# Kernel optimization log

Hardware: AMD Instinct MI355X
Metric: run time of the kernel (lower is better)

The kernel has to match this reference:

```python
import jax, jax.numpy as jnp
import numpy as np

DIM = 128
H = W = 56
NUM_HEADS = 4
WS = 7            # window size
SHIFT = 3
N = WS * WS       # tokens per window (49)
EPS = 1e-5


def _relative_position_index():
    coords = np.stack(np.meshgrid(np.arange(WS), np.arange(WS), indexing='ij'))  # [2,ws,ws]
    cf = coords.reshape(2, -1)                                                   # [2,N]
    rel = cf[:, :, None] - cf[:, None, :]                                        # [2,N,N]
    rel = rel.transpose(1, 2, 0).astype(np.int64)                                # [N,N,2]
    rel[:, :, 0] += WS - 1
    rel[:, :, 1] += WS - 1
    rel[:, :, 0] *= 2 * WS - 1
    return rel.sum(-1)  # [N,N]


def _attn_mask():
    # shifted-window attention mask, [nW, N, N] with 0 / -100
    img = np.zeros((H, W), dtype=np.float32)
    cnt = 0
    for hs in (slice(0, -WS), slice(-WS, -SHIFT), slice(-SHIFT, None)):
        for ws_ in (slice(0, -WS), slice(-WS, -SHIFT), slice(-SHIFT, None)):
            img[hs, ws_] = cnt
            cnt += 1
    mw = img.reshape(H // WS, WS, W // WS, WS).transpose(0, 2, 1, 3).reshape(-1, N)  # [nW,N]
    diff = mw[:, None, :] - mw[:, :, None]
    return np.where(diff != 0, -100.0, 0.0).astype(np.float32)


_RPI = jnp.asarray(_relative_position_index())
_MASK = jnp.asarray(_attn_mask())


def _layernorm(x, g, b):
    mu = jnp.mean(x, axis=-1, keepdims=True)
    var = jnp.mean(jnp.square(x - mu), axis=-1, keepdims=True)
    return (x - mu) * jax.lax.rsqrt(var + EPS) * g + b


def _window_partition(x):
    # x: [B,H,W,C] -> [B*nW, N, C]
    B, _, _, C = x.shape
    x = x.reshape(B, H // WS, WS, W // WS, WS, C).transpose(0, 1, 3, 2, 4, 5)
    return x.reshape(-1, N, C)


def _window_reverse(w, B):
    # [B*nW, N, C] -> [B,H,W,C]
    C = w.shape[-1]
    x = w.reshape(B, H // WS, W // WS, WS, WS, C).transpose(0, 1, 3, 2, 4, 5)
    return x.reshape(B, H, W, C)


def setup_inputs() -> dict:
    key = jax.random.key(0)
    ks = jax.random.split(key, 8)
    B, L, C = 64, H * W, DIM
    hid = 4 * DIM
    s = 0.02
    return {
        'x': jax.random.normal(ks[0], (B, L, C), jnp.float32),
        'norm1_g': jnp.ones((C,), jnp.float32),
        'norm1_b': jnp.zeros((C,), jnp.float32),
        'qkv_w': jax.random.normal(ks[1], (C, 3 * C), jnp.float32) * s,
        'qkv_b': jnp.zeros((3 * C,), jnp.float32),
        'rel_bias_table': jax.random.normal(ks[2], ((2 * WS - 1) ** 2, NUM_HEADS), jnp.float32) * s,
        'proj_w': jax.random.normal(ks[3], (C, C), jnp.float32) * s,
        'proj_b': jnp.zeros((C,), jnp.float32),
        'norm2_g': jnp.ones((C,), jnp.float32),
        'norm2_b': jnp.zeros((C,), jnp.float32),
        'fc1_w': jax.random.normal(ks[4], (C, hid), jnp.float32) * s,
        'fc1_b': jnp.zeros((hid,), jnp.float32),
        'fc2_w': jax.random.normal(ks[5], (hid, C), jnp.float32) * s,
        'fc2_b': jnp.zeros((C,), jnp.float32),
    }


def reference(x, norm1_g, norm1_b, qkv_w, qkv_b, rel_bias_table, proj_w, proj_b,
              norm2_g, norm2_b, fc1_w, fc1_b, fc2_w, fc2_b):
    B, L, C = x.shape
    hdim = C // NUM_HEADS
    scale = hdim ** -0.5

    shortcut = x
    xn = _layernorm(x, norm1_g, norm1_b).reshape(B, H, W, C)

    # cyclic shift (H,W divisible by WS -> no padding)
    xs = jnp.roll(xn, shift=(-SHIFT, -SHIFT), axis=(1, 2))
    xw = _window_partition(xs)                      # [B*nW, N, C]
    B_ = xw.shape[0]
    nW = B_ // B

    # window attention
    qkv = xw @ qkv_w + qkv_b                        # [B_,N,3C]
    qkv = qkv.reshape(B_, N, 3, NUM_HEADS, hdim).transpose(2, 0, 3, 1, 4)
    q, k, v = qkv[0], qkv[1], qkv[2]                # [B_,h,N,d]
    attn = jnp.einsum('bhnd,bhmd->bhnm', q * scale, k)
    bias = rel_bias_table[_RPI.reshape(-1)].reshape(N, N, NUM_HEADS)
    attn = attn + bias.transpose(2, 0, 1)[None]
    attn = attn.reshape(B, nW, NUM_HEADS, N, N) + _MASK[None, :, None]
    attn = jax.nn.softmax(attn.reshape(B_, NUM_HEADS, N, N), axis=-1)
    out = jnp.einsum('bhnm,bhmd->bhnd', attn, v)
    out = out.transpose(0, 2, 1, 3).reshape(B_, N, C)
    out = out @ proj_w + proj_b

    # reverse windows, un-shift
    xr = _window_reverse(out, B)
    xr = jnp.roll(xr, shift=(SHIFT, SHIFT), axis=(1, 2))
    x = shortcut + xr.reshape(B, L, C)

    # MLP with exact GELU (torch nn.GELU default)
    xn2 = _layernorm(x, norm2_g, norm2_b)
    h = jax.nn.gelu(xn2 @ fc1_w + fc1_b, approximate=False)
    x = x + (h @ fc2_w + fc2_b)
    return x
```

## Files before the change

kernel.cpp:

```cpp
#include <hip/hip_runtime.h>
#include <cstdint>

#define DIM   128
#define NH    4
#define WSZ   7
#define NTOK  49
#define SHIFT 3
#define HIMG  56
#define BATCH 64
#define LTOK  3136
#define HID   512
#define EPSF  1e-5f

typedef short bf16x8 __attribute__((ext_vector_type(8)));
typedef float f32x4  __attribute__((ext_vector_type(4)));

__device__ __forceinline__ float bf2f(ushort u){ return __uint_as_float(((uint32_t)u)<<16); }
__device__ __forceinline__ ushort f2bf(float f){
  uint32_t u = __float_as_uint(f);
  u += 0x7FFFu + ((u>>16)&1u);
  return (ushort)(u>>16);
}

__device__ __forceinline__ float gelu_f(float v){
  float xa = fabsf(v) * 0.70710678118654752f;
  float t  = __builtin_amdgcn_rcpf(fmaf(0.3275911f, xa, 1.0f));
  float p  = fmaf(fmaf(fmaf(fmaf(1.061405429f, t, -1.453152027f), t,
                       1.421413741f), t, -0.284496736f), t, 0.254829592f) * t;
  float e  = __expf(-xa*xa);
  float er = copysignf(fmaf(-p, e, 1.0f), v);
  return 0.5f * v * (1.0f + er);
}

__global__ __launch_bounds__(256) void transpose_cvt_all(
    const float* __restrict__ qkvw, const float* __restrict__ pw,
    const float* __restrict__ f1w,  const float* __restrict__ f2w,
    ushort* __restrict__ ws)
{
  __shared__ ushort tile[32][33];
  int bid = blockIdx.x;
  const float* src; ushort* dst; int R, Cc, b0;
  if (bid < 48)       { src = qkvw; dst = ws;          R = 128; Cc = 384; b0 = 0;   }
  else if (bid < 64)  { src = pw;   dst = ws + 49152;  R = 128; Cc = 128; b0 = 48;  }
  else if (bid < 128) { src = f1w;  dst = ws + 65536;  R = 128; Cc = 512; b0 = 64;  }
  else                { src = f2w;  dst = ws + 131072; R = 512; Cc = 128; b0 = 128; }
  int t = bid - b0;
  int tpr = Cc >> 5;
  int tr = t / tpr, tc = t % tpr;
  int tx = threadIdx.x & 31, ty = threadIdx.x >> 5;
  #pragma unroll
  for (int k = 0; k < 4; k++){
    int r = tr*32 + ty + k*8;
    tile[ty + k*8][tx] = f2bf(src[(size_t)r*Cc + tc*32 + tx]);
  }
  __syncthreads();
  #pragma unroll
  for (int k = 0; k < 4; k++){
    int c = tc*32 + ty + k*8;
    dst[(size_t)c*R + tr*32 + tx] = tile[tx][ty + k*8];
  }
}

#define OFF_BUFA 0
#define OFF_QK   8704
#define QKSTR    40
#define OFF_TBL  (OFF_QK + 8*NTOK*QKSTR)
#define OFF_PP   (OFF_QK + 12936)
#define SMEM_SZ  25072

__global__ __launch_bounds__(256,3) void swin_block_kernel(
    const float* __restrict__ x, const float* __restrict__ n1g, const float* __restrict__ n1b,
    const ushort* __restrict__ qkv_wt, const float* __restrict__ qkvb,
    const float* __restrict__ bias_tbl, const ushort* __restrict__ proj_wt,
    const float* __restrict__ projb,
    const float* __restrict__ n2g, const float* __restrict__ n2b,
    const ushort* __restrict__ fc1_wt, const float* __restrict__ fc1b,
    const ushort* __restrict__ fc2_wt, const float* __restrict__ fc2b,
    float* __restrict__ out)
{
  __shared__ ushort smem[SMEM_SZ];

  const int tid  = threadIdx.x;
  const int wave = tid >> 6;
  const int lane = tid & 63;
  const int b_   = blockIdx.x;
  const int b    = b_ >> 6;
  const int win  = b_ & 63;
  const int wi   = win >> 3, wj = win & 7;

  const int ncol  = lane & 15;
  const int quad  = lane >> 4;
  const int koff  = quad * 8;
  const int rbase = quad * 4;
  const int l32   = lane & 31;
  const int hlf   = lane >> 5;

  for (int i = tid; i < 676; i += 256) smem[OFF_TBL + i] = f2bf(bias_tbl[i]);

  {
    const int c = l32*4;
    const float4 g4 = *(const float4*)(n1g + c);
    const float4 b4 = *(const float4*)(n1b + c);
    for (int r = wave*2 + hlf; r < NTOK; r += 8){
      int ti = r / 7, tj = r % 7;
      int hh = (wi*7 + ti + SHIFT) % HIMG;
      int ww = (wj*7 + tj + SHIFT) % HIMG;
      float4 tv = *(const float4*)(x + ((size_t)b*LTOK + hh*HIMG + ww)*DIM + c);
      float sm = tv.x + tv.y + tv.z + tv.w;
      #pragma unroll
      for (int off=16; off; off>>=1) sm += __shfl_xor(sm, off, 64);
      float mu = sm * (1.0f/128.0f);
      float d0 = tv.x-mu, d1 = tv.y-mu, d2 = tv.z-mu, d3 = tv.w-mu;
      float sq = d0*d0 + d1*d1 + d2*d2 + d3*d3;
      #pragma unroll
      for (int off=16; off; off>>=1) sq += __shfl_xor(sq, off, 64);
      float rstd = rsqrtf(sq*(1.0f/128.0f) + EPSF);
      ushort4 o;
      o.x = f2bf(d0*rstd*g4.x + b4.x);
      o.y = f2bf(d1*rstd*g4.y + b4.y);
      o.z = f2bf(d2*rstd*g4.z + b4.z);
      o.w = f2bf(d3*rstd*g4.w + b4.w);
      *(ushort4*)&smem[OFF_BUFA + r*136 + c] = o;
    }
  }
  __syncthreads();

  {
    bf16x8 afrag[4][4];
    #pragma unroll
    for (int mt=0; mt<4; mt++)
      #pragma unroll
      for (int kb=0; kb<4; kb++)
        afrag[mt][kb] = *(const bf16x8*)&smem[OFF_BUFA + (mt*16 + ncol)*136 + kb*32 + koff];
    __syncthreads();

    for (int i = tid; i < 128*15; i += 256){
      int dd = i/15, t = 49 + i%15;
      smem[OFF_BUFA + dd*68 + t] = 0;
    }

    #pragma unroll
    for (int nt=0; nt<6; nt++){
      int c = wave*96 + nt*16 + ncol;
      int which = c >> 7, head = (c >> 5) & 3, d = c & 31;
      bf16x8 bfrag[4];
      #pragma unroll
      for (int kb=0; kb<4; kb++) bfrag[kb] = *(const bf16x8*)(qkv_wt + (size_t)c*128 + kb*32 + koff);
      float bias = qkvb[c];
      int qkb = OFF_QK + (head*2 + which)*NTOK*QKSTR + d;
      int vb  = OFF_BUFA + (head*32 + d)*68;
      #pragma unroll
      for (int mt=0; mt<4; mt++){
        f32x4 acc = {0.f,0.f,0.f,0.f};
        #pragma unroll
        for (int kb=0; kb<4; kb++)
          acc = __builtin_amdgcn_mfma_f32_16x16x32_bf16(afrag[mt][kb], bfrag[kb], acc, 0,0,0);
        #pragma unroll
        for (int r=0; r<4; r++){
          int m = mt*16 + rbase + r;
          if (m < NTOK){
            ushort v = f2bf(acc[r] + bias);
            if (which == 2) smem[vb + m] = v;
            else            smem[qkb + m*QKSTR] = v;
          }
        }
      }
    }
  }
  __syncthreads();

  float4 xpre[7];

  {
    const int h = wave;
    const int qbase = OFF_QK + (h*2    )*NTOK*QKSTR;
    const int kbase = OFF_QK + (h*2 + 1)*NTOK*QKSTR;
    const int pbase = qbase;

    bf16x8 qf[4], kf[4];
    #pragma unroll
    for (int mt=0; mt<4; mt++) qf[mt] = *(const bf16x8*)&smem[qbase + (mt*16 + ncol)*QKSTR + koff];
    #pragma unroll
    for (int nt=0; nt<4; nt++) kf[nt] = *(const bf16x8*)&smem[kbase + (nt*16 + ncol)*QKSTR + koff];

    f32x4 s[4][4];
    #pragma unroll
    for (int mt=0; mt<4; mt++)
      #pragma unroll
      for (int nt=0; nt<4; nt++){
        f32x4 z = {0.f,0.f,0.f,0.f};
        s[mt][nt] = __builtin_amdgcn_mfma_f32_16x16x32_bf16(qf[mt], kf[nt], z, 0,0,0);
      }

    int kcol[4], rm[4];
    #pragma unroll
    for (int nt=0; nt<4; nt++){
      int k = nt*16 + ncol;
      kcol[nt] = k;
      int kc = k < NTOK ? k : 48;
      int si = kc/7, sj = kc%7;
      int sh = wi*7 + si, sw = wj*7 + sj;
      rm[nt] = (sh<49?0:(sh<53?1:2))*3 + (sw<49?0:(sw<53?1:2));
    }
    const float scale = 0.17677669529663687f;

    #pragma unroll
    for (int mt=0; mt<4; mt++){
      #pragma unroll
      for (int r=0; r<4; r++){
        int m  = mt*16 + rbase + r;
        int mc = m < NTOK ? m : 48;
        int ti = mc/7, tj = mc%7;
        int habs = wi*7 + ti, wabs = wj*7 + tj;
        int rn = (habs<49?0:(habs<53?1:2))*3 + (wabs<49?0:(wabs<53?1:2));
        float sv[4];
        #pragma unroll
        for (int nt=0; nt<4; nt++){
          int k  = kcol[nt];
          int kc = k < NTOK ? k : 48;
          int si = kc/7, sj = kc%7;
          int idx = (ti - si + 6)*13 + (tj - sj + 6);
          float bias = bf2f(smem[OFF_TBL + idx*4 + h]);
          float v = s[mt][nt][r]*scale + bias + (rn == rm[nt] ? 0.f : -100.f);
          sv[nt] = (k < NTOK) ? v : -1e30f;
        }
        float sum = 0.f;
        #pragma unroll
        for (int nt=0; nt<4; nt++){ sv[nt] = __expf(sv[nt]); sum += sv[nt]; }
        #pragma unroll
        for (int off=1; off<16; off<<=1) sum += __shfl_xor(sum, off, 64);
        float rs = 1.0f/sum;
        #pragma unroll
        for (int nt=0; nt<4; nt++) s[mt][nt][r] = sv[nt]*rs;
      }
    }

    #pragma unroll
    for (int kk=0; kk<7; kk++){
      int rr = wave*2 + hlf + kk*8;
      if (rr < NTOK){
        int ti = rr/7, tj = rr%7;
        int hh = (wi*7 + ti + SHIFT) % HIMG;
        int ww = (wj*7 + tj + SHIFT) % HIMG;
        xpre[kk] = *(const float4*)(x + ((size_t)b*LTOK + hh*HIMG + ww)*DIM + l32*4);
      }
    }

    #pragma unroll
    for (int mt=0; mt<4; mt++)
      #pragma unroll
      for (int r=0; r<4; r++){
        int m = mt*16 + rbase + r;
        if (m < NTOK){
          #pragma unroll
          for (int nt=0; nt<4; nt++)
            smem[pbase + m*72 + kcol[nt]] = f2bf(s[mt][nt][r]);
        }
      }

    bf16x8 vf[2][2];
    #pragma unroll
    for (int nt=0; nt<2; nt++)
      #pragma unroll
      for (int kq=0; kq<2; kq++)
        vf[nt][kq] = *(const bf16x8*)&smem[OFF_BUFA + (h*32 + nt*16 + ncol)*68 + kq*32 + koff];
    __syncthreads();

    f32x4 o[4][2];
    #pragma unroll
    for (int mt=0; mt<4; mt++)
      #pragma unroll
      for (int nt=0; nt<2; nt++){ f32x4 z={0.f,0.f,0.f,0.f}; o[mt][nt]=z; }

    #pragma unroll
    for (int mt=0; mt<4; mt++)
      #pragma unroll
      for (int kq=0; kq<2; kq++){
        bf16x8 pf = *(const bf16x8*)&smem[pbase + (mt*16 + ncol)*72 + kq*32 + koff];
        #pragma unroll
        for (int nt=0; nt<2; nt++)
          o[mt][nt] = __builtin_amdgcn_mfma_f32_16x16x32_bf16(pf, vf[nt][kq], o[mt][nt], 0,0,0);
      }

    #pragma unroll
    for (int mt=0; mt<4; mt++)
      #pragma unroll
      for (int nt=0; nt<2; nt++)
        #pragma unroll
        for (int r=0; r<4; r++){
          int m = mt*16 + rbase + r;
          if (m < NTOK)
            smem[OFF_BUFA + m*136 + h*32 + nt*16 + ncol] = f2bf(o[mt][nt][r]);
        }
  }
  __syncthreads();

  float* xstage = (float*)&smem[OFF_QK];
  #pragma unroll
  for (int kk=0; kk<7; kk++){
    int rr = wave*2 + hlf + kk*8;
    if (rr < NTOK) *(float4*)&xstage[rr*132 + l32*4] = xpre[kk];
  }

  float x2reg[2][4][4];
  {
    bf16x8 afrag[4][4];
    #pragma unroll
    for (int mt=0; mt<4; mt++)
      #pragma unroll
      for (int kb=0; kb<4; kb++)
        afrag[mt][kb] = *(const bf16x8*)&smem[OFF_BUFA + (mt*16 + ncol)*136 + kb*32 + koff];
    __syncthreads();

    #pragma unroll
    for (int nt=0; nt<2; nt++){
      int j = wave*32 + nt*16 + ncol;
      bf16x8 bfrag[4];
      #pragma unroll
      for (int kb=0; kb<4; kb++) bfrag[kb] = *(const bf16x8*)(proj_wt + (size_t)j*128 + kb*32 + koff);
      float bias = projb[j];
      #pragma unroll
      for (int mt=0; mt<4; mt++){
        f32x4 acc = {0.f,0.f,0.f,0.f};
        #pragma unroll
        for (int kb=0; kb<4; kb++)
          acc = __builtin_amdgcn_mfma_f32_16x16x32_bf16(afrag[mt][kb], bfrag[kb], acc, 0,0,0);
        #pragma unroll
        for (int r=0; r<4; r++){
          int m = mt*16 + rbase + r;
          if (m < NTOK) x2reg[nt][mt][r] = acc[r] + bias + xstage[m*132 + j];
          else          x2reg[nt][mt][r] = 0.f;
        }
      }
    }
  }

  float2* pp = (float2*)&smem[OFF_PP];
  #pragma unroll
  for (int mt=0; mt<4; mt++)
    #pragma unroll
    for (int r=0; r<4; r++){
      float a0 = x2reg[0][mt][r], a1 = x2reg[1][mt][r];
      float sm = a0 + a1, sq = a0*a0 + a1*a1;
      #pragma unroll
      for (int off=1; off<16; off<<=1){ sm += __shfl_xor(sm, off, 64); sq += __shfl_xor(sq, off, 64); }
      if (ncol == 0) pp[(mt*16 + rbase + r)*4 + wave] = make_float2(sm, sq);
    }
  __syncthreads();

  {
    const int j0 = wave*32 + ncol, j1 = j0 + 16;
    const float g0 = n2g[j0], be0 = n2b[j0], g1 = n2g[j1], be1 = n2b[j1];
    #pragma unroll
    for (int mt=0; mt<4; mt++)
      #pragma unroll
      for (int r=0; r<4; r++){
        int m = mt*16 + rbase + r;
        f32x4 pa = *(const f32x4*)&pp[m*4];
        f32x4 pb = *(const f32x4*)&pp[m*4 + 2];
        float sm = pa[0]+pa[2]+pb[0]+pb[2];
        float sq = pa[1]+pa[3]+pb[1]+pb[3];
        float mu   = sm * (1.0f/128.0f);
        float rstd = rsqrtf(sq*(1.0f/128.0f) - mu*mu + EPSF);
        smem[OFF_BUFA + m*136 + j0] = f2bf((x2reg[0][mt][r]-mu)*rstd*g0 + be0);
        smem[OFF_BUFA + m*136 + j1] = f2bf((x2reg[1][mt][r]-mu)*rstd*g1 + be1);
      }
  }
  __syncthreads();

  f32x4 o2[2][4];
  #pragma unroll
  for (int nt=0; nt<2; nt++)
    #pragma unroll
    for (int mt=0; mt<4; mt++){ f32x4 z={0.f,0.f,0.f,0.f}; o2[nt][mt]=z; }

  for (int hk=0; hk<4; hk++){
    {
      bf16x8 bfrag2[2][4];
      float  bias2[2];
      #pragma unroll
      for (int nt=0; nt<2; nt++){
        int c = hk*128 + wave*32 + nt*16 + ncol;
        #pragma unroll
        for (int kb=0; kb<4; kb++)
          bfrag2[nt][kb] = *(const bf16x8*)(fc1_wt + (size_t)c*128 + kb*32 + koff);
        bias2[nt] = fc1b[c];
      }
      #pragma unroll
      for (int mt=0; mt<4; mt++){
        bf16x8 a4[4];
        #pragma unroll
        for (int kb=0; kb<4; kb++)
          a4[kb] = *(const bf16x8*)&smem[OFF_BUFA + (mt*16 + ncol)*136 + kb*32 + koff];
        #pragma unroll
        for (int nt=0; nt<2; nt++){
          f32x4 acc = {0.f,0.f,0.f,0.f};
          #pragma unroll
          for (int kb=0; kb<4; kb++)
            acc = __builtin_amdgcn_mfma_f32_16x16x32_bf16(a4[kb], bfrag2[nt][kb], acc, 0,0,0);
          int cloc = wave*32 + nt*16 + ncol;
          #pragma unroll
          for (int r=0; r<4; r++){
            int m = mt*16 + rbase + r;
            if (mt < 3 || m < NTOK)
              smem[OFF_QK + m*136 + cloc] = f2bf(gelu_f(acc[r] + bias2[nt]));
          }
        }
      }
    }
    __syncthreads();

    {
      bf16x8 bfrag2[2][4];
      #pragma unroll
      for (int nt=0; nt<2; nt++){
        int j = wave*32 + nt*16 + ncol;
        #pragma unroll
        for (int kb=0; kb<4; kb++)
          bfrag2[nt][kb] = *(const bf16x8*)(fc2_wt + (size_t)j*512 + hk*128 + kb*32 + koff);
      }
      #pragma unroll
      for (int mt=0; mt<4; mt++){
        bf16x8 ha4[4];
        #pragma unroll
        for (int kb=0; kb<4; kb++)
          ha4[kb] = *(const bf16x8*)&smem[OFF_QK + (mt*16 + ncol)*136 + kb*32 + koff];
        #pragma unroll
        for (int nt=0; nt<2; nt++)
          #pragma unroll
          for (int kb=0; kb<4; kb++)
            o2[nt][mt] = __builtin_amdgcn_mfma_f32_16x16x32_bf16(ha4[kb], bfrag2[nt][kb], o2[nt][mt], 0,0,0);
      }
    }
    __syncthreads();
  }

  float* fout = (float*)&smem[OFF_QK];
  #pragma unroll
  for (int nt=0; nt<2; nt++){
    int j = wave*32 + nt*16 + ncol;
    float bias = fc2b[j];
    #pragma unroll
    for (int mt=0; mt<4; mt++){
      #pragma unroll
      for (int r=0; r<4; r++){
        int m = mt*16 + rbase + r;
        if (m < NTOK)
          fout[m*132 + j] = o2[nt][mt][r] + bias + x2reg[nt][mt][r];
      }
    }
  }
  __syncthreads();

  for (int rr = wave*2 + hlf; rr < NTOK; rr += 8){
    int ti = rr/7, tj = rr%7;
    int hh = (wi*7 + ti + SHIFT) % HIMG;
    int ww = (wj*7 + tj + SHIFT) % HIMG;
    float4 v = *(const float4*)&fout[rr*132 + l32*4];
    *(float4*)(out + ((size_t)b*LTOK + hh*HIMG + ww)*DIM + l32*4) = v;
  }
}

extern "C" void kernel_launch(void* const* d_in, const int* in_sizes, int n_in,
                              void* d_out, int out_size, void* d_ws, size_t ws_size,
                              hipStream_t stream)
{
  const float* x    = (const float*)d_in[0];
  const float* n1g  = (const float*)d_in[1];
  const float* n1b  = (const float*)d_in[2];
  const float* qkvw = (const float*)d_in[3];
  const float* qkvb = (const float*)d_in[4];
  const float* tbl  = (const float*)d_in[5];
  const float* pw   = (const float*)d_in[6];
  const float* pb   = (const float*)d_in[7];
  const float* n2g  = (const float*)d_in[8];
  const float* n2b  = (const float*)d_in[9];
  const float* f1w  = (const float*)d_in[10];
  const float* f1b  = (const float*)d_in[11];
  const float* f2w  = (const float*)d_in[12];
  const float* f2b  = (const float*)d_in[13];

  ushort* wsbase = (ushort*)d_ws;
  transpose_cvt_all<<<192, 256, 0, stream>>>(qkvw, pw, f1w, f2w, wsbase);

  swin_block_kernel<<<4096, 256, 0, stream>>>(x, n1g, n1b, wsbase, qkvb, tbl,
                                              wsbase + 49152, pb, n2g, n2b,
                                              wsbase + 65536, f1b, wsbase + 131072, f2b,
                                              (float*)d_out);
}
```

Measured before the change: 486.9 us.

## Prefetch weight fragments early and simplify softmax bias/exp computation

Global weight fragments for the QKV, proj, fc1 and fc2 GEMMs are now loaded ahead of use: before barriers, one tile ahead in loops, or at the start of each MLP chunk. This hides global-load latency behind MFMA work and synchronisation. The relative-position bias table is stored in fp32 prescaled by log2(e), so softmax uses a single fma and exp2 with a precomputed index offset instead of per-element index arithmetic and bf16 decode. The residual x prefetch is moved before the softmax. The cost is more live registers under launch_bounds(256,3), which risks spills, plus slightly more shared memory.

```diff
diff --git a/kernel.cpp b/kernel.cpp
--- a/kernel.cpp
+++ b/kernel.cpp
@@ -15,7 +15,6 @@
 typedef short bf16x8 __attribute__((ext_vector_type(8)));
 typedef float f32x4  __attribute__((ext_vector_type(4)));
 
-__device__ __forceinline__ float bf2f(ushort u){ return __uint_as_float(((uint32_t)u)<<16); }
 __device__ __forceinline__ ushort f2bf(float f){
   uint32_t u = __float_as_uint(f);
   u += 0x7FFFu + ((u>>16)&1u);
@@ -66,7 +65,7 @@
 #define QKSTR    40
 #define OFF_TBL  (OFF_QK + 8*NTOK*QKSTR)
 #define OFF_PP   (OFF_QK + 12936)
-#define SMEM_SZ  25072
+#define SMEM_SZ  25744
 
 __global__ __launch_bounds__(256,3) void swin_block_kernel(
     const float* __restrict__ x, const float* __restrict__ n1g, const float* __restrict__ n1b,
@@ -95,7 +94,10 @@
   const int l32   = lane & 31;
   const int hlf   = lane >> 5;
 
-  for (int i = tid; i < 676; i += 256) smem[OFF_TBL + i] = f2bf(bias_tbl[i]);
+  {
+    float* tblI = (float*)&smem[OFF_TBL];
+    for (int i = tid; i < 676; i += 256) tblI[i] = bias_tbl[i] * 1.4426950408889634f;
+  }
 
   {
     const int c = l32*4;
@@ -123,6 +125,14 @@
       *(ushort4*)&smem[OFF_BUFA + r*136 + c] = o;
     }
   }
+
+  bf16x8 bfp[4];
+  {
+    int c0 = wave*96 + ncol;
+    #pragma unroll
+    for (int kb=0; kb<4; kb++)
+      bfp[kb] = *(const bf16x8*)(qkv_wt + (size_t)c0*128 + kb*32 + koff);
+  }
   __syncthreads();
 
   {
@@ -142,10 +152,16 @@
     #pragma unroll
     for (int nt=0; nt<6; nt++){
       int c = wave*96 + nt*16 + ncol;
+      bf16x8 bfrag[4];
+      #pragma unroll
+      for (int kb=0; kb<4; kb++) bfrag[kb] = bfp[kb];
+      if (nt < 5){
+        int cn = c + 16;
+        #pragma unroll
+        for (int kb=0; kb<4; kb++)
+          bfp[kb] = *(const bf16x8*)(qkv_wt + (size_t)cn*128 + kb*32 + koff);
+      }
       int which = c >> 7, head = (c >> 5) & 3, d = c & 31;
-      bf16x8 bfrag[4];
-      #pragma unroll
-      for (int kb=0; kb<4; kb++) bfrag[kb] = *(const bf16x8*)(qkv_wt + (size_t)c*128 + kb*32 + koff);
       float bias = qkvb[c];
       int qkb = OFF_QK + (head*2 + which)*NTOK*QKSTR + d;
       int vb  = OFF_BUFA + (head*32 + d)*68;
@@ -192,7 +208,18 @@
         s[mt][nt] = __builtin_amdgcn_mfma_f32_16x16x32_bf16(qf[mt], kf[nt], z, 0,0,0);
       }
 
-    int kcol[4], rm[4];
+    #pragma unroll
+    for (int kk=0; kk<7; kk++){
+      int rr = wave*2 + hlf + kk*8;
+      if (rr < NTOK){
+        int ti = rr/7, tj = rr%7;
+        int hh = (wi*7 + ti + SHIFT) % HIMG;
+        int ww = (wj*7 + tj + SHIFT) % HIMG;
+        xpre[kk] = *(const float4*)(x + ((size_t)b*LTOK + hh*HIMG + ww)*DIM + l32*4);
+      }
+    }
+
+    int kcol[4], rm[4], offI[4];
     #pragma unroll
     for (int nt=0; nt<4; nt++){
       int k = nt*16 + ncol;
@@ -201,8 +228,11 @@
       int si = kc/7, sj = kc%7;
       int sh = wi*7 + si, sw = wj*7 + sj;
       rm[nt] = (sh<49?0:(sh<53?1:2))*3 + (sw<49?0:(sw<53?1:2));
-    }
-    const float scale = 0.17677669529663687f;
+      offI[nt] = (si*13 + sj)*4;
+    }
+    const float* tblF = (const float*)&smem[OFF_TBL];
+    const float SCL2 = 0.25503486f;
+    const float MASK_L2E = -144.26950408889634f;
 
     #pragma unroll
     for (int mt=0; mt<4; mt++){
@@ -213,36 +243,22 @@
         int ti = mc/7, tj = mc%7;
         int habs = wi*7 + ti, wabs = wj*7 + tj;
         int rn = (habs<49?0:(habs<53?1:2))*3 + (wabs<49?0:(wabs<53?1:2));
+        int baseI = (ti*13 + tj + 84)*4 + h;
         float sv[4];
         #pragma unroll
         for (int nt=0; nt<4; nt++){
-          int k  = kcol[nt];
-          int kc = k < NTOK ? k : 48;
-          int si = kc/7, sj = kc%7;
-          int idx = (ti - si + 6)*13 + (tj - sj + 6);
-          float bias = bf2f(smem[OFF_TBL + idx*4 + h]);
-          float v = s[mt][nt][r]*scale + bias + (rn == rm[nt] ? 0.f : -100.f);
-          sv[nt] = (k < NTOK) ? v : -1e30f;
+          float bias = tblF[baseI - offI[nt]];
+          float v = fmaf(s[mt][nt][r], SCL2, bias) + (rn == rm[nt] ? 0.f : MASK_L2E);
+          sv[nt] = (kcol[nt] < NTOK) ? v : -1e30f;
         }
         float sum = 0.f;
         #pragma unroll
-        for (int nt=0; nt<4; nt++){ sv[nt] = __expf(sv[nt]); sum += sv[nt]; }
+        for (int nt=0; nt<4; nt++){ sv[nt] = __builtin_amdgcn_exp2f(sv[nt]); sum += sv[nt]; }
         #pragma unroll
         for (int off=1; off<16; off<<=1) sum += __shfl_xor(sum, off, 64);
         float rs = 1.0f/sum;
         #pragma unroll
         for (int nt=0; nt<4; nt++) s[mt][nt][r] = sv[nt]*rs;
-      }
-    }
-
-    #pragma unroll
-    for (int kk=0; kk<7; kk++){
-      int rr = wave*2 + hlf + kk*8;
-      if (rr < NTOK){
-        int ti = rr/7, tj = rr%7;
-        int hh = (wi*7 + ti + SHIFT) % HIMG;
-        int ww = (wj*7 + tj + SHIFT) % HIMG;
-        xpre[kk] = *(const float4*)(x + ((size_t)b*LTOK + hh*HIMG + ww)*DIM + l32*4);
       }
     }
 
@@ -302,6 +318,15 @@
     if (rr < NTOK) *(float4*)&xstage[rr*132 + l32*4] = xpre[kk];
   }
 
+  bf16x8 pbf[2][4];
+  #pragma unroll
+  for (int nt=0; nt<2; nt++){
+    int j = wave*32 + nt*16 + ncol;
+    #pragma unroll
+    for (int kb=0; kb<4; kb++)
+      pbf[nt][kb] = *(const bf16x8*)(proj_wt + (size_t)j*128 + kb*32 + koff);
+  }
+
   float x2reg[2][4][4];
   {
     bf16x8 afrag[4][4];
@@ -315,16 +340,13 @@
     #pragma unroll
     for (int nt=0; nt<2; nt++){
       int j = wave*32 + nt*16 + ncol;
-      bf16x8 bfrag[4];
-      #pragma unroll
-      for (int kb=0; kb<4; kb++) bfrag[kb] = *(const bf16x8*)(proj_wt + (size_t)j*128 + kb*32 + koff);
       float bias = projb[j];
       #pragma unroll
       for (int mt=0; mt<4; mt++){
         f32x4 acc = {0.f,0.f,0.f,0.f};
         #pragma unroll
         for (int kb=0; kb<4; kb++)
-          acc = __builtin_amdgcn_mfma_f32_16x16x32_bf16(afrag[mt][kb], bfrag[kb], acc, 0,0,0);
+          acc = __builtin_amdgcn_mfma_f32_16x16x32_bf16(afrag[mt][kb], pbf[nt][kb], acc, 0,0,0);
         #pragma unroll
         for (int r=0; r<4; r++){
           int m = mt*16 + rbase + r;
@@ -347,6 +369,15 @@
       if (ncol == 0) pp[(mt*16 + rbase + r)*4 + wave] = make_float2(sm, sq);
     }
   __syncthreads();
+
+  bf16x8 f1p[2][4];
+  #pragma unroll
+  for (int nt=0; nt<2; nt++){
+    int c = wave*32 + nt*16 + ncol;
+    #pragma unroll
+    for (int kb=0; kb<4; kb++)
+      f1p[nt][kb] = *(const bf16x8*)(fc1_wt + (size_t)c*128 + kb*32 + koff);
+  }
 
   {
     const int j0 = wave*32 + ncol, j1 = j0 + 16;
@@ -375,17 +406,19 @@
     for (int mt=0; mt<4; mt++){ f32x4 z={0.f,0.f,0.f,0.f}; o2[nt][mt]=z; }
 
   for (int hk=0; hk<4; hk++){
+    bf16x8 f2p[2][4];
+    #pragma unroll
+    for (int nt=0; nt<2; nt++){
+      int j = wave*32 + nt*16 + ncol;
+      #pragma unroll
+      for (int kb=0; kb<4; kb++)
+        f2p[nt][kb] = *(const bf16x8*)(fc2_wt + (size_t)j*512 + hk*128 + kb*32 + koff);
+    }
+
     {
-      bf16x8 bfrag2[2][4];
-      float  bias2[2];
-      #pragma unroll
-      for (int nt=0; nt<2; nt++){
-        int c = hk*128 + wave*32 + nt*16 + ncol;
-        #pragma unroll
-        for (int kb=0; kb<4; kb++)
-          bfrag2[nt][kb] = *(const bf16x8*)(fc1_wt + (size_t)c*128 + kb*32 + koff);
-        bias2[nt] = fc1b[c];
-      }
+      float bias2[2];
+      #pragma unroll
+      for (int nt=0; nt<2; nt++) bias2[nt] = fc1b[hk*128 + wave*32 + nt*16 + ncol];
       #pragma unroll
       for (int mt=0; mt<4; mt++){
         bf16x8 a4[4];
@@ -397,7 +430,7 @@
           f32x4 acc = {0.f,0.f,0.f,0.f};
           #pragma unroll
           for (int kb=0; kb<4; kb++)
-            acc = __builtin_amdgcn_mfma_f32_16x16x32_bf16(a4[kb], bfrag2[nt][kb], acc, 0,0,0);
+            acc = __builtin_amdgcn_mfma_f32_16x16x32_bf16(a4[kb], f1p[nt][kb], acc, 0,0,0);
           int cloc = wave*32 + nt*16 + ncol;
           #pragma unroll
           for (int r=0; r<4; r++){
@@ -408,29 +441,28 @@
         }
       }
     }
+    if (hk < 3){
+      #pragma unroll
+      for (int nt=0; nt<2; nt++){
+        int c = (hk+1)*128 + wave*32 + nt*16 + ncol;
+        #pragma unroll
+        for (int kb=0; kb<4; kb++)
+          f1p[nt][kb] = *(const bf16x8*)(fc1_wt + (size_t)c*128 + kb*32 + koff);
+      }
+    }
     __syncthreads();
 
-    {
-      bf16x8 bfrag2[2][4];
-      #pragma unroll
-      for (int nt=0; nt<2; nt++){
-        int j = wave*32 + nt*16 + ncol;
+    #pragma unroll
+    for (int mt=0; mt<4; mt++){
+      bf16x8 ha4[4];
+      #pragma unroll
+      for (int kb=0; kb<4; kb++)
+        ha4[kb] = *(const bf16x8*)&smem[OFF_QK + (mt*16 + ncol)*136 + kb*32 + koff];
+      #pragma unroll
+      for (int nt=0; nt<2; nt++)
         #pragma unroll
         for (int kb=0; kb<4; kb++)
-          bfrag2[nt][kb] = *(const bf16x8*)(fc2_wt + (size_t)j*512 + hk*128 + kb*32 + koff);
-      }
-      #pragma unroll
-      for (int mt=0; mt<4; mt++){
-        bf16x8 ha4[4];
-        #pragma unroll
-        for (int kb=0; kb<4; kb++)
-          ha4[kb] = *(const bf16x8*)&smem[OFF_QK + (mt*16 + ncol)*136 + kb*32 + koff];
-        #pragma unroll
-        for (int nt=0; nt<2; nt++)
-          #pragma unroll
-          for (int kb=0; kb<4; kb++)
-            o2[nt][mt] = __builtin_amdgcn_mfma_f32_16x16x32_bf16(ha4[kb], bfrag2[nt][kb], o2[nt][mt], 0,0,0);
-      }
+          o2[nt][mt] = __builtin_amdgcn_mfma_f32_16x16x32_bf16(ha4[kb], f2p[nt][kb], o2[nt][mt], 0,0,0);
     }
     __syncthreads();
   }
```

New measurement: 521.2 us. 1.07x slower.
